# Kernel optimization log

Hardware: AMD Instinct MI355X
Metric: run time of the kernel (lower is better)

The kernel has to match this reference:

```python
import jax, jax.numpy as jnp
import numpy as np

N_NODES = 200_000
N_EDGES = 6_400_000
N_GRAPHS = 512


def _sage_conv(x, edge_index, Wl, bl, Wr):
    """PyG SAGEConv (mean aggr): lin_l(mean_j x_j) + lin_r(x_i).
    lin_l has bias, lin_r does not. Messages flow src -> dst."""
    src, dst = edge_index[0], edge_index[1]
    n = x.shape[0]
    # gather neighbor features [E, F] and segment-mean into dst nodes
    msg_sum = jax.ops.segment_sum(x[src], dst, num_segments=n)
    deg = jax.ops.segment_sum(jnp.ones((src.shape[0],), x.dtype), dst, num_segments=n)
    mean = msg_sum / jnp.maximum(deg, 1.0)[:, None]  # zero in-degree -> 0
    return mean @ Wl.T + bl + x @ Wr.T


def setup_inputs() -> dict:
    key = jax.random.key(0)
    ks = jax.random.split(key, 9)
    x = jax.random.normal(ks[0], (N_NODES, 1), dtype=jnp.float32)
    edge_index = jax.random.randint(ks[1], (2, N_EDGES), 0, N_NODES, dtype=jnp.int64)
    batch = jnp.sort(jax.random.randint(ks[2], (N_NODES,), 0, N_GRAPHS, dtype=jnp.int64))
    W1l = jax.random.normal(ks[3], (16, 1), dtype=jnp.float32)
    b1 = jax.random.normal(ks[4], (16,), dtype=jnp.float32)
    W1r = jax.random.normal(ks[5], (16, 1), dtype=jnp.float32)
    W2l = jax.random.normal(ks[6], (1, 16), dtype=jnp.float32)
    b2 = jax.random.normal(ks[7], (1,), dtype=jnp.float32)
    W2r = jax.random.normal(ks[8], (1, 16), dtype=jnp.float32)
    return {"x": x, "edge_index": edge_index, "batch": batch, "batch_size": N_GRAPHS,
            "W1l": W1l, "b1": b1, "W1r": W1r, "W2l": W2l, "b2": b2, "W2r": W2r}


def reference(x, edge_index, batch, batch_size, W1l, b1, W1r, W2l, b2, W2r):
    h = _sage_conv(x, edge_index, W1l, b1, W1r)          # [N, 16]
    h = jax.nn.relu(h)
    h = _sage_conv(h, edge_index, W2l, b2, W2r)          # [N, 1]
    # global_add_pool: segment-sum node features by graph id
    out = jax.ops.segment_sum(h, batch, num_segments=batch_size)  # [B, 1]
    return out
```

## Files before the change

### kernel.cpp

```cpp
#include <hip/hip_runtime.h>


#define BLK       1024
#define TILE      (BLK * 4)
#define NSB       25
#define SBSH      13
#define WMSK      8191u
#define RING      32u
#define RMSK      31u
#define MAXC      512
#define TPAD      16
#define CNT_ONE   (1u << 25)
#define FX_BIAS   131072
#define SCALE     4096.0f
#define INV_SCALE (1.0f / 4096.0f)
#define IDQ       8388608.0f

__global__ __launch_bounds__(BLK) void partition_kernel(
    const int* __restrict__ ei, const float* __restrict__ x,
    unsigned* __restrict__ xq1, unsigned* __restrict__ pairs,
    unsigned* __restrict__ tails, int E, int N, int bins, unsigned Mdiv,
    int capC, int nc) {
    extern __shared__ unsigned buf[];
    __shared__ unsigned cnt[MAXC], base[MAXC], fq[MAXC], gb[MAXC];
    const int tid = threadIdx.x;
    for (int j = tid; j < nc; j += BLK) { cnt[j] = 0; base[j] = 0; }

    for (int n = blockIdx.x * BLK + tid; n < N; n += gridDim.x * BLK)
        xq1[n] = CNT_ONE + (unsigned)((int)rintf(x[n] * SCALE) + FX_BIAS);
    __syncthreads();

    const int ntiles = (E + TILE - 1) / TILE;
    for (int t = blockIdx.x; t < ntiles; t += gridDim.x) {
        int e0 = t * TILE + tid * 4;
        int nv = E - e0; nv = nv < 0 ? 0 : (nv > 4 ? 4 : nv);
        int srcv[4], dstv[4];
        if (nv == 4 && ((E & 3) == 0)) {
            int4 s = *(const int4*)(ei + e0);
            int4 d = *(const int4*)(ei + E + e0);
            srcv[0] = s.x; srcv[1] = s.y; srcv[2] = s.z; srcv[3] = s.w;
            dstv[0] = d.x; dstv[1] = d.y; dstv[2] = d.z; dstv[3] = d.w;
        } else {
            for (int j = 0; j < nv; ++j) { srcv[j] = ei[e0 + j]; dstv[j] = ei[E + e0 + j]; }
        }
        unsigned w[4]; int cell[4]; bool pend[4];
        for (int j = 0; j < 4; ++j) {
            pend[j] = (j < nv);
            if (pend[j]) {
                unsigned dst = (unsigned)dstv[j];
                unsigned src = (unsigned)srcv[j];
                unsigned pt = (unsigned)(((unsigned long long)dst * Mdiv) >> 32);
                int ld = (int)dst - (int)pt * bins;
                while (ld >= bins) { ld -= bins; ++pt; }
                while (ld < 0)     { ld += bins; --pt; }
                cell[j] = (int)(pt * NSB + (src >> SBSH));
                w[j] = ((src & WMSK) << 14) | (unsigned)ld;
            }
        }
        for (int j = 0; j < 4; ++j) {
            if (pend[j]) {
                unsigned slot = atomicAdd(&cnt[cell[j]], 1u);
                if (slot - base[cell[j]] < RING) {
                    buf[cell[j] * RING + (slot & RMSK)] = w[j]; pend[j] = false;
                } else atomicSub(&cnt[cell[j]], 1u);
            }
        }
        int npend = __syncthreads_count((int)(pend[0] | pend[1] | pend[2] | pend[3]));
        while (npend > 0) {
            for (int j = tid; j < nc; j += BLK) {
                unsigned avail = cnt[j] - base[j];
                unsigned f = avail & ~RMSK;
                fq[j] = f;
                if (f) gb[j] = atomicAdd(&tails[(size_t)j * TPAD], f);
            }
            __syncthreads();
            {
                int wv = tid >> 6, lane = tid & 63;
                for (int r = wv; r < nc; r += 16) {
                    unsigned f = fq[r];
                    if (f) {
                        unsigned g0 = gb[r], bs = base[r];
                        unsigned mx = (g0 + f <= (unsigned)capC) ? f : ((unsigned)capC > g0 ? (unsigned)capC - g0 : 0u);
                        unsigned* dp = pairs + (size_t)r * capC + g0;
                        for (unsigned jj = lane; jj < mx; jj += 64)
                            dp[jj] = buf[r * RING + ((bs + jj) & RMSK)];
                    }
                }
            }
            __syncthreads();
            for (int j = tid; j < nc; j += BLK) base[j] += fq[j];
            __syncthreads();
            for (int j = 0; j < 4; ++j) {
                if (pend[j]) {
                    unsigned slot = atomicAdd(&cnt[cell[j]], 1u);
                    if (slot - base[cell[j]] < RING) {
                        buf[cell[j] * RING + (slot & RMSK)] = w[j]; pend[j] = false;
                    } else atomicSub(&cnt[cell[j]], 1u);
                }
            }
            npend = __syncthreads_count((int)(pend[0] | pend[1] | pend[2] | pend[3]));
        }
    }
    for (int j = tid; j < nc; j += BLK) {
        unsigned avail = cnt[j] - base[j];
        fq[j] = avail;
        if (avail) gb[j] = atomicAdd(&tails[(size_t)j * TPAD], avail);
    }
    __syncthreads();
    {
        int wv = tid >> 6, lane = tid & 63;
        for (int r = wv; r < nc; r += 16) {
            unsigned f = fq[r];
            if (f) {
                unsigned g0 = gb[r], bs = base[r];
                unsigned mx = (g0 + f <= (unsigned)capC) ? f : ((unsigned)capC > g0 ? (unsigned)capC - g0 : 0u);
                unsigned* dp = pairs + (size_t)r * capC + g0;
                for (unsigned jj = lane; jj < mx; jj += 64)
                    dp[jj] = buf[r * RING + ((bs + jj) & RMSK)];
            }
        }
    }
}

__global__ __launch_bounds__(BLK, 8) void bin1_kernel(
    const unsigned* __restrict__ pairs, const unsigned* __restrict__ tails,
    const unsigned* __restrict__ xq1, unsigned* __restrict__ slab,
    int N, int bins, int capC) {
    extern __shared__ unsigned sm[];
    unsigned* xs = sm;
    unsigned* sb = sm + 8192;
    const int tid = threadIdx.x;
    const int cell = blockIdx.x;
    const int p = cell / NSB;
    const int sbk = cell - p * NSB;
    const int wb = sbk << SBSH;
    int nn = N - wb; if (nn > 8192) nn = 8192;
    for (int j = tid; j < nn; j += BLK) xs[j] = xq1[wb + j];
    for (int j = tid; j < bins; j += BLK) sb[j] = 0;
    __syncthreads();
    int len = (int)tails[(size_t)cell * TPAD]; if (len > capC) len = capC;
    const unsigned* bp = pairs + (size_t)cell * capC;
    int len4 = len & ~3;
    const uint4* bp4 = (const uint4*)bp;
    for (int e = tid; e < (len4 >> 2); e += BLK) {
        uint4 wq = bp4[e];
        atomicAdd(&sb[wq.x & 16383u], xs[wq.x >> 14]);
        atomicAdd(&sb[wq.y & 16383u], xs[wq.y >> 14]);
        atomicAdd(&sb[wq.z & 16383u], xs[wq.z >> 14]);
        atomicAdd(&sb[wq.w & 16383u], xs[wq.w >> 14]);
    }
    for (int e = len4 + tid; e < len; e += BLK) {
        unsigned wv = bp[e];
        atomicAdd(&sb[wv & 16383u], xs[wv >> 14]);
    }
    __syncthreads();
    unsigned* dst = slab + (size_t)sbk * N + (size_t)p * bins;
    int nb = N - p * bins; if (nb > bins) nb = bins;
    for (int j = tid; j < nb; j += BLK) dst[j] = sb[j];
}

__global__ void node_pass1_kernel(const float* __restrict__ x,
                                  const unsigned* __restrict__ slab,
                                  const float* __restrict__ W1l,
                                  const float* __restrict__ b1,
                                  const float* __restrict__ W1r,
                                  const float* __restrict__ W2l,
                                  const float* __restrict__ W2r,
                                  const float* __restrict__ b2,
                                  const int* __restrict__ batch,
                                  int* __restrict__ pvq,
                                  unsigned* __restrict__ zd,
                                  float* __restrict__ out,
                                  int N) {
    __shared__ float s_w1l[16], s_b1[16], s_w1r[16], s_w2l[16], s_w2r[16];
    if (threadIdx.x < 16) {
        s_w1l[threadIdx.x] = W1l[threadIdx.x];
        s_b1[threadIdx.x]  = b1[threadIdx.x];
        s_w1r[threadIdx.x] = W1r[threadIdx.x];
        s_w2l[threadIdx.x] = W2l[threadIdx.x];
        s_w2r[threadIdx.x] = W2r[threadIdx.x];
    }
    __syncthreads();
    int n = blockIdx.x * blockDim.x + threadIdx.x;
    float b2v = b2[0];
    float val = 0.0f;
    int g;
    if (n < N) {
        unsigned cnt = 0, fx = 0;
#pragma unroll
        for (int c = 0; c < NSB; ++c) {
            unsigned w = slab[(size_t)c * N + n];
            cnt += w >> 25;
            fx  += w & (CNT_ONE - 1);
        }
        float dg  = (float)cnt;
        float sum = (float)(int)(fx - cnt * (unsigned)FX_BIAS) * INV_SCALE;
        float m   = sum / fmaxf(dg, 1.0f);

        float xv = x[n];
        float pa = 0.0f, qa = 0.0f;
#pragma unroll
        for (int f = 0; f < 16; ++f) {
            float h = fmaf(m, s_w1l[f], fmaf(xv, s_w1r[f], s_b1[f]));
            h = fmaxf(h, 0.0f);
            pa = fmaf(h, s_w2l[f], pa);
            qa = fmaf(h, s_w2r[f], qa);
        }
        pvq[n] = (int)rintf(pa * SCALE);
        float invd = 1.0f / fmaxf(dg, 1.0f);
        unsigned q = (unsigned)rintf(invd * IDQ);
        if (q > 8388607u) q = 8388607u;
        g = batch[n];
        zd[n] = ((unsigned)g << 23) | q;
        val = qa + b2v;
    } else {
        g = batch[N - 1];
    }
    int g0 = __shfl(g, 0);
    unsigned long long same = __ballot(g == g0);
    if (same == ~0ULL) {
        for (int off = 32; off > 0; off >>= 1) val += __shfl_down(val, off);
        if ((threadIdx.x & 63) == 0) atomicAdd(&out[g0], val);
    } else {
        atomicAdd(&out[g], val);
    }
}

__global__ __launch_bounds__(BLK, 8) void pool_kernel(
    const unsigned* __restrict__ pairs, const unsigned* __restrict__ tails,
    const int* __restrict__ pvq, const unsigned* __restrict__ zd,
    unsigned long long* __restrict__ outq,
    int N, int bins, int capC) {
    extern __shared__ unsigned sm[];
    int* ps = (int*)sm;
    unsigned* zs = sm + 8192;
    unsigned long long* gbin =
        (unsigned long long*)(sm + 8192 + 10000);
    const int tid = threadIdx.x;
    const int cell = blockIdx.x;
    const int p = cell / NSB;
    const int sbk = cell - p * NSB;
    const int wb = sbk << SBSH;
    int nn = N - wb; if (nn > 8192) nn = 8192;
    for (int j = tid; j < nn; j += BLK) ps[j] = pvq[wb + j];
    int nb = N - p * bins; if (nb > bins) nb = bins;
    for (int j = tid; j < nb; j += BLK) zs[j] = zd[(size_t)p * bins + j];
    if (tid < 512) gbin[tid] = 0ULL;
    __syncthreads();
    int len = (int)tails[(size_t)cell * TPAD]; if (len > capC) len = capC;
    const unsigned* bp = pairs + (size_t)cell * capC;
    int len4 = len & ~3;
    const uint4* bp4 = (const uint4*)bp;
    for (int e = tid; e < (len4 >> 2); e += BLK) {
        uint4 wq = bp4[e];
        {
            unsigned z = zs[wq.x & 16383u];
            int t = (int)rintf((float)ps[wq.x >> 14] *
                               ((float)(z & 0x7FFFFFu) * (1.0f / IDQ)));
            atomicAdd(&gbin[z >> 23], (unsigned long long)(long long)t);
        }
        {
            unsigned z = zs[wq.y & 16383u];
            int t = (int)rintf((float)ps[wq.y >> 14] *
                               ((float)(z & 0x7FFFFFu) * (1.0f / IDQ)));
            atomicAdd(&gbin[z >> 23], (unsigned long long)(long long)t);
        }
        {
            unsigned z = zs[wq.z & 16383u];
            int t = (int)rintf((float)ps[wq.z >> 14] *
                               ((float)(z & 0x7FFFFFu) * (1.0f / IDQ)));
            atomicAdd(&gbin[z >> 23], (unsigned long long)(long long)t);
        }
        {
            unsigned z = zs[wq.w & 16383u];
            int t = (int)rintf((float)ps[wq.w >> 14] *
                               ((float)(z & 0x7FFFFFu) * (1.0f / IDQ)));
            atomicAdd(&gbin[z >> 23], (unsigned long long)(long long)t);
        }
    }
    for (int e = len4 + tid; e < len; e += BLK) {
        unsigned wv = bp[e];
        unsigned z = zs[wv & 16383u];
        int t = (int)rintf((float)ps[wv >> 14] *
                           ((float)(z & 0x7FFFFFu) * (1.0f / IDQ)));
        atomicAdd(&gbin[z >> 23], (unsigned long long)(long long)t);
    }
    __syncthreads();
    if (tid < 512) {
        unsigned long long v = gbin[tid];
        if (v) atomicAdd(&outq[tid], v);
    }
}

__global__ void finalize_kernel(const unsigned long long* __restrict__ outq,
                                float* __restrict__ out, int B) {
    int g = blockIdx.x * blockDim.x + threadIdx.x;
    if (g < B)
        out[g] += (float)(long long)outq[g] * INV_SCALE;
}

extern "C" void kernel_launch(void* const* d_in, const int* in_sizes, int n_in,
                              void* d_out, int out_size, void* d_ws, size_t ws_size,
                              hipStream_t stream) {
    const float* x     = (const float*)d_in[0];
    const int*   ei    = (const int*)d_in[1];
    const int*   batch = (const int*)d_in[2];
    const float* W1l = (const float*)d_in[4];
    const float* b1  = (const float*)d_in[5];
    const float* W1r = (const float*)d_in[6];
    const float* W2l = (const float*)d_in[7];
    const float* b2  = (const float*)d_in[8];
    const float* W2r = (const float*)d_in[9];

    const int N = in_sizes[0];
    const int E = in_sizes[1] / 2;
    float* out = (float*)d_out;

    const int pp   = 20;
    const int bins = (N + pp - 1) / pp;
    const int nc   = pp * NSB;
    const unsigned Mdiv =
        (unsigned)(((1ULL << 32) + (unsigned)bins - 1) / (unsigned)bins);
    long long cellExp = ((long long)E / pp) * 8192 / N;
    int capC = (int)((cellExp + 2048 + 1023) & ~1023LL);

    unsigned* pairs = (unsigned*)d_ws;
    unsigned* slab1 = pairs + (size_t)nc * capC;
    int*      pvq   = (int*)(slab1 + (size_t)NSB * N);
    unsigned* zd    = (unsigned*)(pvq + N);
    unsigned* xq1   = zd + N;
    unsigned* tails = xq1 + N;
    unsigned long long* outq =
        (unsigned long long*)(tails + (size_t)nc * TPAD);

    hipMemsetAsync(d_out, 0, (size_t)out_size * sizeof(float), stream);
    hipMemsetAsync(tails, 0,
                   ((size_t)nc * TPAD + 1024) * sizeof(unsigned), stream);

    const int partShmem = nc * (int)RING * 4;
    const int binShmem  = (8192 + bins) * 4;
    const int poolShmem = (8192 + bins) * 4 + 512 * 8;
    hipFuncSetAttribute((const void*)partition_kernel,
                        hipFuncAttributeMaxDynamicSharedMemorySize, partShmem);
    hipFuncSetAttribute((const void*)bin1_kernel,
                        hipFuncAttributeMaxDynamicSharedMemorySize, binShmem);
    hipFuncSetAttribute((const void*)pool_kernel,
                        hipFuncAttributeMaxDynamicSharedMemorySize, poolShmem);

    const int partBlocks = 512;
    const int NB = 256;
    int node_blocks = (N + NB - 1) / NB;

    partition_kernel<<<partBlocks, BLK, partShmem, stream>>>(ei, x, xq1, pairs,
                                                             tails, E, N, bins,
                                                             Mdiv, capC, nc);
    bin1_kernel<<<nc, BLK, binShmem, stream>>>(pairs, tails, xq1, slab1,
                                               N, bins, capC);
    node_pass1_kernel<<<node_blocks, NB, 0, stream>>>(x, slab1, W1l, b1, W1r,
                                                      W2l, W2r, b2, batch,
                                                      pvq, zd, out, N);
    pool_kernel<<<nc, BLK, poolShmem, stream>>>(pairs, tails, pvq, zd, outq,
                                                N, bins, capC);
    finalize_kernel<<<(out_size + 255) / 256, 256, 0, stream>>>(outq, out,
                                                                out_size);
}
```

Before: 212.8 us.

## Replace shared-memory ring-buffer partitioning with per-block private bucket slots

```diff
diff --git a/kernel.cpp b/kernel.cpp
--- a/kernel.cpp
+++ b/kernel.cpp
@@ -3,13 +3,12 @@
 
 #define BLK       1024
 #define TILE      (BLK * 4)
+#define NBLK      512
+#define CAPB      128
 #define NSB       25
 #define SBSH      13
 #define WMSK      8191u
-#define RING      32u
-#define RMSK      31u
-#define MAXC      512
-#define TPAD      16
+#define OVFCAP    (1u << 21)
 #define CNT_ONE   (1u << 25)
 #define FX_BIAS   131072
 #define SCALE     4096.0f
@@ -19,19 +18,20 @@
 __global__ __launch_bounds__(BLK) void partition_kernel(
     const int* __restrict__ ei, const float* __restrict__ x,
     unsigned* __restrict__ xq1, unsigned* __restrict__ pairs,
-    unsigned* __restrict__ tails, int E, int N, int bins, unsigned Mdiv,
-    int capC, int nc) {
-    extern __shared__ unsigned buf[];
-    __shared__ unsigned cnt[MAXC], base[MAXC], fq[MAXC], gb[MAXC];
+    unsigned* __restrict__ blockCnt, unsigned long long* __restrict__ ovf,
+    unsigned* __restrict__ ovfTail, int E, int N, int bins, unsigned Mdiv,
+    int nc) {
+    __shared__ unsigned cur[NBLK];
     const int tid = threadIdx.x;
-    for (int j = tid; j < nc; j += BLK) { cnt[j] = 0; base[j] = 0; }
-
-    for (int n = blockIdx.x * BLK + tid; n < N; n += gridDim.x * BLK)
+    const unsigned bid = blockIdx.x;
+    for (int j = tid; j < nc; j += BLK) cur[j] = 0;
+
+    for (int n = (int)bid * BLK + tid; n < N; n += NBLK * BLK)
         xq1[n] = CNT_ONE + (unsigned)((int)rintf(x[n] * SCALE) + FX_BIAS);
     __syncthreads();
 
     const int ntiles = (E + TILE - 1) / TILE;
-    for (int t = blockIdx.x; t < ntiles; t += gridDim.x) {
+    for (int t = (int)bid; t < ntiles; t += NBLK) {
         int e0 = t * TILE + tid * 4;
         int nv = E - e0; nv = nv < 0 ? 0 : (nv > 4 ? 4 : nv);
         int srcv[4], dstv[4];
@@ -43,92 +43,44 @@
         } else {
             for (int j = 0; j < nv; ++j) { srcv[j] = ei[e0 + j]; dstv[j] = ei[E + e0 + j]; }
         }
-        unsigned w[4]; int cell[4]; bool pend[4];
         for (int j = 0; j < 4; ++j) {
-            pend[j] = (j < nv);
-            if (pend[j]) {
+            if (j < nv) {
                 unsigned dst = (unsigned)dstv[j];
                 unsigned src = (unsigned)srcv[j];
                 unsigned pt = (unsigned)(((unsigned long long)dst * Mdiv) >> 32);
                 int ld = (int)dst - (int)pt * bins;
                 while (ld >= bins) { ld -= bins; ++pt; }
                 while (ld < 0)     { ld += bins; --pt; }
-                cell[j] = (int)(pt * NSB + (src >> SBSH));
-                w[j] = ((src & WMSK) << 14) | (unsigned)ld;
-            }
-        }
-        for (int j = 0; j < 4; ++j) {
-            if (pend[j]) {
-                unsigned slot = atomicAdd(&cnt[cell[j]], 1u);
-                if (slot - base[cell[j]] < RING) {
-                    buf[cell[j] * RING + (slot & RMSK)] = w[j]; pend[j] = false;
-                } else atomicSub(&cnt[cell[j]], 1u);
-            }
-        }
-        int npend = __syncthreads_count((int)(pend[0] | pend[1] | pend[2] | pend[3]));
-        while (npend > 0) {
-            for (int j = tid; j < nc; j += BLK) {
-                unsigned avail = cnt[j] - base[j];
-                unsigned f = avail & ~RMSK;
-                fq[j] = f;
-                if (f) gb[j] = atomicAdd(&tails[(size_t)j * TPAD], f);
-            }
-            __syncthreads();
-            {
-                int wv = tid >> 6, lane = tid & 63;
-                for (int r = wv; r < nc; r += 16) {
-                    unsigned f = fq[r];
-                    if (f) {
-                        unsigned g0 = gb[r], bs = base[r];
-                        unsigned mx = (g0 + f <= (unsigned)capC) ? f : ((unsigned)capC > g0 ? (unsigned)capC - g0 : 0u);
-                        unsigned* dp = pairs + (size_t)r * capC + g0;
-                        for (unsigned jj = lane; jj < mx; jj += 64)
-                            dp[jj] = buf[r * RING + ((bs + jj) & RMSK)];
-                    }
+                unsigned cell = pt * NSB + (src >> SBSH);
+                unsigned w = ((src & WMSK) << 14) | (unsigned)ld;
+                unsigned idx = atomicAdd(&cur[cell], 1u);
+                if (idx < CAPB) {
+                    pairs[((((size_t)cell << 9) | bid) << 7) + idx] = w;
+                } else {
+                    unsigned ot = atomicAdd(ovfTail, 1u);
+                    if (ot < OVFCAP)
+                        ovf[ot] = ((unsigned long long)cell << 32) | w;
                 }
             }
-            __syncthreads();
-            for (int j = tid; j < nc; j += BLK) base[j] += fq[j];
-            __syncthreads();
-            for (int j = 0; j < 4; ++j) {
-                if (pend[j]) {
-                    unsigned slot = atomicAdd(&cnt[cell[j]], 1u);
-                    if (slot - base[cell[j]] < RING) {
-                        buf[cell[j] * RING + (slot & RMSK)] = w[j]; pend[j] = false;
-                    } else atomicSub(&cnt[cell[j]], 1u);
-                }
-            }
-            npend = __syncthreads_count((int)(pend[0] | pend[1] | pend[2] | pend[3]));
-        }
-    }
+        }
+    }
+    __syncthreads();
     for (int j = tid; j < nc; j += BLK) {
-        unsigned avail = cnt[j] - base[j];
-        fq[j] = avail;
-        if (avail) gb[j] = atomicAdd(&tails[(size_t)j * TPAD], avail);
-    }
-    __syncthreads();
-    {
-        int wv = tid >> 6, lane = tid & 63;
-        for (int r = wv; r < nc; r += 16) {
-            unsigned f = fq[r];
-            if (f) {
-                unsigned g0 = gb[r], bs = base[r];
-                unsigned mx = (g0 + f <= (unsigned)capC) ? f : ((unsigned)capC > g0 ? (unsigned)capC - g0 : 0u);
-                unsigned* dp = pairs + (size_t)r * capC + g0;
-                for (unsigned jj = lane; jj < mx; jj += 64)
-                    dp[jj] = buf[r * RING + ((bs + jj) & RMSK)];
-            }
-        }
+        unsigned c = cur[j]; if (c > CAPB) c = CAPB;
+        blockCnt[((size_t)j << 9) | bid] = c;
     }
 }
 
 __global__ __launch_bounds__(BLK, 8) void bin1_kernel(
-    const unsigned* __restrict__ pairs, const unsigned* __restrict__ tails,
+    const unsigned* __restrict__ pairs, const unsigned* __restrict__ blockCnt,
+    const unsigned long long* __restrict__ ovf,
+    const unsigned* __restrict__ ovfTail,
     const unsigned* __restrict__ xq1, unsigned* __restrict__ slab,
-    int N, int bins, int capC) {
+    int N, int bins) {
     extern __shared__ unsigned sm[];
     unsigned* xs = sm;
     unsigned* sb = sm + 8192;
+    __shared__ unsigned scnt[NBLK];
     const int tid = threadIdx.x;
     const int cell = blockIdx.x;
     const int p = cell / NSB;
@@ -137,21 +89,28 @@
     int nn = N - wb; if (nn > 8192) nn = 8192;
     for (int j = tid; j < nn; j += BLK) xs[j] = xq1[wb + j];
     for (int j = tid; j < bins; j += BLK) sb[j] = 0;
-    __syncthreads();
-    int len = (int)tails[(size_t)cell * TPAD]; if (len > capC) len = capC;
-    const unsigned* bp = pairs + (size_t)cell * capC;
-    int len4 = len & ~3;
-    const uint4* bp4 = (const uint4*)bp;
-    for (int e = tid; e < (len4 >> 2); e += BLK) {
-        uint4 wq = bp4[e];
-        atomicAdd(&sb[wq.x & 16383u], xs[wq.x >> 14]);
-        atomicAdd(&sb[wq.y & 16383u], xs[wq.y >> 14]);
-        atomicAdd(&sb[wq.z & 16383u], xs[wq.z >> 14]);
-        atomicAdd(&sb[wq.w & 16383u], xs[wq.w >> 14]);
-    }
-    for (int e = len4 + tid; e < len; e += BLK) {
-        unsigned wv = bp[e];
-        atomicAdd(&sb[wv & 16383u], xs[wv >> 14]);
+    for (int j = tid; j < NBLK; j += BLK) scnt[j] = blockCnt[((size_t)cell << 9) + j];
+    __syncthreads();
+    {
+        int wv6 = tid >> 6, lane = tid & 63;
+        for (int s = wv6; s < NBLK; s += 16) {
+            int len = (int)scnt[s];
+            const unsigned* sp = pairs + ((((size_t)cell << 9) | (unsigned)s) << 7);
+            for (int jj = lane; jj < len; jj += 64) {
+                unsigned w = sp[jj];
+                atomicAdd(&sb[w & 16383u], xs[w >> 14]);
+            }
+        }
+    }
+    {
+        unsigned ot = *ovfTail; if (ot > OVFCAP) ot = OVFCAP;
+        for (unsigned e = tid; e < ot; e += BLK) {
+            unsigned long long pk = ovf[e];
+            if ((unsigned)(pk >> 32) == (unsigned)cell) {
+                unsigned w = (unsigned)pk;
+                atomicAdd(&sb[w & 16383u], xs[w >> 14]);
+            }
+        }
     }
     __syncthreads();
     unsigned* dst = slab + (size_t)sbk * N + (size_t)p * bins;
@@ -227,15 +186,18 @@
 }
 
 __global__ __launch_bounds__(BLK, 8) void pool_kernel(
-    const unsigned* __restrict__ pairs, const unsigned* __restrict__ tails,
+    const unsigned* __restrict__ pairs, const unsigned* __restrict__ blockCnt,
+    const unsigned long long* __restrict__ ovf,
+    const unsigned* __restrict__ ovfTail,
     const int* __restrict__ pvq, const unsigned* __restrict__ zd,
     unsigned long long* __restrict__ outq,
-    int N, int bins, int capC) {
+    int N, int bins) {
     extern __shared__ unsigned sm[];
     int* ps = (int*)sm;
     unsigned* zs = sm + 8192;
     unsigned long long* gbin =
         (unsigned long long*)(sm + 8192 + 10000);
+    __shared__ unsigned scnt[NBLK];
     const int tid = threadIdx.x;
     const int cell = blockIdx.x;
     const int p = cell / NSB;
@@ -245,45 +207,35 @@
     for (int j = tid; j < nn; j += BLK) ps[j] = pvq[wb + j];
     int nb = N - p * bins; if (nb > bins) nb = bins;
     for (int j = tid; j < nb; j += BLK) zs[j] = zd[(size_t)p * bins + j];
+    for (int j = tid; j < NBLK; j += BLK) scnt[j] = blockCnt[((size_t)cell << 9) + j];
     if (tid < 512) gbin[tid] = 0ULL;
     __syncthreads();
-    int len = (int)tails[(size_t)cell * TPAD]; if (len > capC) len = capC;
-    const unsigned* bp = pairs + (size_t)cell * capC;
-    int len4 = len & ~3;
-    const uint4* bp4 = (const uint4*)bp;
-    for (int e = tid; e < (len4 >> 2); e += BLK) {
-        uint4 wq = bp4[e];
-        {
-            unsigned z = zs[wq.x & 16383u];
-            int t = (int)rintf((float)ps[wq.x >> 14] *
-                               ((float)(z & 0x7FFFFFu) * (1.0f / IDQ)));
-            atomicAdd(&gbin[z >> 23], (unsigned long long)(long long)t);
-        }
-        {
-            unsigned z = zs[wq.y & 16383u];
-            int t = (int)rintf((float)ps[wq.y >> 14] *
-                               ((float)(z & 0x7FFFFFu) * (1.0f / IDQ)));
-            atomicAdd(&gbin[z >> 23], (unsigned long long)(long long)t);
-        }
-        {
-            unsigned z = zs[wq.z & 16383u];
-            int t = (int)rintf((float)ps[wq.z >> 14] *
-                               ((float)(z & 0x7FFFFFu) * (1.0f / IDQ)));
-            atomicAdd(&gbin[z >> 23], (unsigned long long)(long long)t);
-        }
-        {
-            unsigned z = zs[wq.w & 16383u];
-            int t = (int)rintf((float)ps[wq.w >> 14] *
-                               ((float)(z & 0x7FFFFFu) * (1.0f / IDQ)));
-            atomicAdd(&gbin[z >> 23], (unsigned long long)(long long)t);
-        }
-    }
-    for (int e = len4 + tid; e < len; e += BLK) {
-        unsigned wv = bp[e];
-        unsigned z = zs[wv & 16383u];
-        int t = (int)rintf((float)ps[wv >> 14] *
-                           ((float)(z & 0x7FFFFFu) * (1.0f / IDQ)));
-        atomicAdd(&gbin[z >> 23], (unsigned long long)(long long)t);
+    {
+        int wv6 = tid >> 6, lane = tid & 63;
+        for (int s = wv6; s < NBLK; s += 16) {
+            int len = (int)scnt[s];
+            const unsigned* sp = pairs + ((((size_t)cell << 9) | (unsigned)s) << 7);
+            for (int jj = lane; jj < len; jj += 64) {
+                unsigned w = sp[jj];
+                unsigned z = zs[w & 16383u];
+                int t = (int)rintf((float)ps[w >> 14] *
+                                   ((float)(z & 0x7FFFFFu) * (1.0f / IDQ)));
+                atomicAdd(&gbin[z >> 23], (unsigned long long)(long long)t);
+            }
+        }
+    }
+    {
+        unsigned ot = *ovfTail; if (ot > OVFCAP) ot = OVFCAP;
+        for (unsigned e = tid; e < ot; e += BLK) {
+            unsigned long long pk = ovf[e];
+            if ((unsigned)(pk >> 32) == (unsigned)cell) {
+                unsigned w = (unsigned)pk;
+                unsigned z = zs[w & 16383u];
+                int t = (int)rintf((float)ps[w >> 14] *
+                                   ((float)(z & 0x7FFFFFu) * (1.0f / IDQ)));
+                atomicAdd(&gbin[z >> 23], (unsigned long long)(long long)t);
+            }
+        }
     }
     __syncthreads();
     if (tid < 512) {
@@ -321,46 +273,41 @@
     const int nc   = pp * NSB;
     const unsigned Mdiv =
         (unsigned)(((1ULL << 32) + (unsigned)bins - 1) / (unsigned)bins);
-    long long cellExp = ((long long)E / pp) * 8192 / N;
-    int capC = (int)((cellExp + 2048 + 1023) & ~1023LL);
 
     unsigned* pairs = (unsigned*)d_ws;
-    unsigned* slab1 = pairs + (size_t)nc * capC;
+    unsigned* slab1 = pairs + (size_t)nc * NBLK * CAPB;
     int*      pvq   = (int*)(slab1 + (size_t)NSB * N);
     unsigned* zd    = (unsigned*)(pvq + N);
     unsigned* xq1   = zd + N;
-    unsigned* tails = xq1 + N;
-    unsigned long long* outq =
-        (unsigned long long*)(tails + (size_t)nc * TPAD);
+    unsigned* blockCnt = xq1 + N;
+    unsigned long long* ovf =
+        (unsigned long long*)(blockCnt + (size_t)nc * NBLK);
+    unsigned* ovfTail = (unsigned*)(ovf + OVFCAP);
+    unsigned long long* outq = (unsigned long long*)(ovfTail + 16);
 
     hipMemsetAsync(d_out, 0, (size_t)out_size * sizeof(float), stream);
-    hipMemsetAsync(tails, 0,
-                   ((size_t)nc * TPAD + 1024) * sizeof(unsigned), stream);
-
-    const int partShmem = nc * (int)RING * 4;
+    hipMemsetAsync(ovfTail, 0, (16 + 1024) * sizeof(unsigned), stream);
+
     const int binShmem  = (8192 + bins) * 4;
     const int poolShmem = (8192 + bins) * 4 + 512 * 8;
-    hipFuncSetAttribute((const void*)partition_kernel,
-                        hipFuncAttributeMaxDynamicSharedMemorySize, partShmem);
     hipFuncSetAttribute((const void*)bin1_kernel,
                         hipFuncAttributeMaxDynamicSharedMemorySize, binShmem);
     hipFuncSetAttribute((const void*)pool_kernel,
                         hipFuncAttributeMaxDynamicSharedMemorySize, poolShmem);
 
-    const int partBlocks = 512;
     const int NB = 256;
     int node_blocks = (N + NB - 1) / NB;
 
-    partition_kernel<<<partBlocks, BLK, partShmem, stream>>>(ei, x, xq1, pairs,
-                                                             tails, E, N, bins,
-                                                             Mdiv, capC, nc);
-    bin1_kernel<<<nc, BLK, binShmem, stream>>>(pairs, tails, xq1, slab1,
-                                               N, bins, capC);
+    partition_kernel<<<NBLK, BLK, 0, stream>>>(ei, x, xq1, pairs, blockCnt,
+                                               ovf, ovfTail, E, N, bins,
+                                               Mdiv, nc);
+    bin1_kernel<<<nc, BLK, binShmem, stream>>>(pairs, blockCnt, ovf, ovfTail,
+                                               xq1, slab1, N, bins);
     node_pass1_kernel<<<node_blocks, NB, 0, stream>>>(x, slab1, W1l, b1, W1r,
                                                       W2l, W2r, b2, batch,
                                                       pvq, zd, out, N);
-    pool_kernel<<<nc, BLK, poolShmem, stream>>>(pairs, tails, pvq, zd, outq,
-                                                N, bins, capC);
+    pool_kernel<<<nc, BLK, poolShmem, stream>>>(pairs, blockCnt, ovf, ovfTail,
+                                                pvq, zd, outq, N, bins);
     finalize_kernel<<<(out_size + 255) / 256, 256, 0, stream>>>(outq, out,
                                                                 out_size);
 }
```

New measurement: 254.8 us. 1.2x slower.
